# Optimization experiments

Measured on AMD Instinct MI355X. Metric: run time of the kernel, lower is better.

The kernel has to match this reference:

```python
import jax, jax.numpy as jnp
import numpy as np

MEMORY_SIZE = 32768
FEATURE_DIM = 128
BATCH = 4096


def setup_inputs() -> dict:
    key = jax.random.key(0)
    k1, k2, k3, k4 = jax.random.split(key, 4)
    memory = jax.random.normal(k1, (MEMORY_SIZE, FEATURE_DIM), dtype=jnp.float32)
    input_data = jax.random.normal(k2, (BATCH, FEATURE_DIM), dtype=jnp.float32)
    write_weights = jax.random.uniform(k3, (BATCH, MEMORY_SIZE), dtype=jnp.float32)
    query = jax.random.normal(k4, (BATCH, FEATURE_DIM), dtype=jnp.float32)
    return {"memory": memory, "input_data": input_data,
            "write_weights": write_weights, "query": query}


def reference(memory, input_data, write_weights, query):
    # ---- write(): row-normalize weights, scatter-accumulate into memory ----
    # The original python double-loop computes update[j] += w[i,j] * x[i],
    # i.e. update = w_norm.T @ x  -- a single GEMM.
    w_norm = write_weights / jnp.sum(write_weights, axis=1, keepdims=True)
    update = jnp.einsum('bm,bf->mf', w_norm, input_data)  # [M, F]
    memory_new = memory + update

    # ---- read(): softmax attention over memory slots ----
    scores = jnp.matmul(query, memory_new.T)              # [B, M]
    attention_weights = jax.nn.softmax(scores, axis=1)
    retrieved_memory = jnp.matmul(attention_weights, memory_new)  # [B, F]
    confidence_scores = jnp.max(attention_weights, axis=1)        # [B]
    return retrieved_memory, confidence_scores, memory_new
```

## Files before the change

kernel.cpp:

```cpp
#include <hip/hip_runtime.h>
#include <hip/hip_bf16.h>
#include <math.h>

#define MEMSZ 32768
#define FDIM  128
#define BATCH 4096

typedef float f32x4 __attribute__((ext_vector_type(4)));
typedef _Float16 f16x8 __attribute__((ext_vector_type(8)));
typedef short bf16x8 __attribute__((ext_vector_type(8)));
typedef unsigned short u16t;
typedef unsigned int u32t;

static __device__ __forceinline__ u16t f2h_bits(float f) {
    union { _Float16 h; u16t u; } c;
    c.h = (_Float16)f;
    return c.u;
}

#define GLDS16(gsrc, ldst) \
  __builtin_amdgcn_global_load_lds((const __attribute__((address_space(1))) void*)(gsrc), \
                                   (__attribute__((address_space(3))) void*)(ldst), 16, 0, 0)

__global__ __launch_bounds__(256) void k_rowsum(const float* __restrict__ W,
                                                float* __restrict__ inv_s) {
    const int row = blockIdx.x;
    const float4* Wr = reinterpret_cast<const float4*>(W + (size_t)row * MEMSZ);
    float acc = 0.f;
    #pragma unroll 4
    for (int i = threadIdx.x; i < MEMSZ / 4; i += 256) {
        float4 v = Wr[i];
        acc += (v.x + v.y) + (v.z + v.w);
    }
    #pragma unroll
    for (int off = 32; off > 0; off >>= 1)
        acc += __shfl_down(acc, off, 64);
    __shared__ float wsum[4];
    const int lane = threadIdx.x & 63, wid = threadIdx.x >> 6;
    if (lane == 0) wsum[wid] = acc;
    __syncthreads();
    if (threadIdx.x == 0)
        inv_s[row] = 1.0f / (wsum[0] + wsum[1] + wsum[2] + wsum[3]);
}

__global__ __launch_bounds__(256) void k_prep(const float* __restrict__ X,
                                              const float* __restrict__ inv_s,
                                              u16t* __restrict__ XT) {
    __shared__ float xs[32][132];
    const int b0 = blockIdx.x * 32;
    const int tid = threadIdx.x;
    #pragma unroll
    for (int i = 0; i < 4; ++i) {
        const int idx = tid + i * 256;
        const int row = idx >> 5, c4 = idx & 31;
        const float s = inv_s[b0 + row];
        float4 v = *reinterpret_cast<const float4*>(&X[(size_t)(b0 + row) * FDIM + c4 * 4]);
        v.x *= s; v.y *= s; v.z *= s; v.w *= s;
        *reinterpret_cast<float4*>(&xs[row][c4 * 4]) = v;
    }
    __syncthreads();
    const int f = tid >> 1, half = tid & 1;
    u32t pk[8];
    #pragma unroll
    for (int h = 0; h < 8; ++h) {
        const float lo = xs[half * 16 + 2 * h][f];
        const float hi = xs[half * 16 + 2 * h + 1][f];
        asm("v_cvt_pk_bf16_f32 %0, %1, %2" : "=v"(pk[h]) : "v"(lo), "v"(hi));
    }
    uint4* dst = reinterpret_cast<uint4*>(XT + (size_t)f * BATCH + b0 + half * 16);
    dst[0] = make_uint4(pk[0], pk[1], pk[2], pk[3]);
    dst[1] = make_uint4(pk[4], pk[5], pk[6], pk[7]);
}

#define K2B 64
#define K2M 128
__global__ __launch_bounds__(512, 2) void k_update_mfma(
    const float* __restrict__ W, const u16t* __restrict__ XT,
    const float* __restrict__ Mem, float* __restrict__ MemNew,
    u16t* __restrict__ MemH, u16t* __restrict__ MemHT)
{
    __shared__ __align__(16) unsigned char wt[2][32768];

    const int tid = threadIdx.x;
    const int lane = tid & 63, w = tid >> 6;
    const int q16 = lane & 15, g = lane >> 4;
    const int wm = w >> 1, wf = w & 1;
    const int mblk = blockIdx.x * K2M;

    f32x4 acc[2][4];
    #pragma unroll
    for (int mf = 0; mf < 2; ++mf)
        #pragma unroll
        for (int ff = 0; ff < 4; ++ff) acc[mf][ff] = (f32x4){0.f, 0.f, 0.f, 0.f};

    auto stage = [&](int buf, int t) {
        const int b0 = t * K2B;
        #pragma unroll
        for (int c = 0; c < 4; ++c) {
            const int gi = c * 512 + tid;
            const int b = gi >> 5;
            const int wb = (gi & 31) * 16;
            const int m4 = wb ^ ((b & 8) << 3);
            GLDS16((const unsigned char*)W + (size_t)(b0 + b) * (MEMSZ * 4) + (size_t)mblk * 4 + m4,
                   &wt[buf][gi * 16]);
        }
    };
    auto loadB = [&](bf16x8 (&br)[4][2], int t) {
        const int b0 = t * K2B;
        #pragma unroll
        for (int ff = 0; ff < 4; ++ff)
            #pragma unroll
            for (int ks = 0; ks < 2; ++ks)
                br[ff][ks] = *reinterpret_cast<const bf16x8*>(
                    XT + (size_t)(wf * 64 + ff * 16 + q16) * BATCH + b0 + ks * 32 + g * 8);
    };
    auto compute = [&](int buf, bf16x8 (&br)[4][2]) {
        bf16x8 afr[2][2];
        const unsigned char* tb = &wt[buf][0];
        const int bm4 = (wm * 32 + q16) * 4;
        #pragma unroll
        for (int mf = 0; mf < 2; ++mf) {
            #pragma unroll
            for (int ks = 0; ks < 2; ++ks) {
                float av[8];
                #pragma unroll
                for (int e = 0; e < 8; ++e)
                    av[e] = *reinterpret_cast<const float*>(
                        tb + (ks * 32 + g * 8 + e) * 512 + ((bm4 + mf * 64) ^ ((g & 1) << 6)));
                union { u32t u[4]; bf16x8 v; } cv;
                #pragma unroll
                for (int h = 0; h < 4; ++h)
                    asm("v_cvt_pk_bf16_f32 %0, %1, %2" : "=v"(cv.u[h]) : "v"(av[2 * h]), "v"(av[2 * h + 1]));
                afr[mf][ks] = cv.v;
            }
        }
        #pragma unroll
        for (int mf = 0; mf < 2; ++mf)
            #pragma unroll
            for (int ff = 0; ff < 4; ++ff)
                #pragma unroll
                for (int ks = 0; ks < 2; ++ks)
                    acc[mf][ff] = __builtin_amdgcn_mfma_f32_16x16x32_bf16(
                        afr[mf][ks], br[ff][ks], acc[mf][ff], 0, 0, 0);
    };

    bf16x8 bE[4][2], bO[4][2];
    stage(0, 0); loadB(bE, 0);
    __syncthreads();
    const int NT = BATCH / K2B;
    for (int t = 0; t < NT; t += 2) {
        stage(1, t + 1); loadB(bO, t + 1);
        compute(0, bE);
        __syncthreads();
        if (t + 2 < NT) { stage(0, t + 2); loadB(bE, t + 2); }
        compute(1, bO);
        __syncthreads();
    }

    #pragma unroll
    for (int mf = 0; mf < 2; ++mf) {
        #pragma unroll
        for (int ff = 0; ff < 4; ++ff) {
            const int m0 = mblk + wm * 32 + mf * 16 + g * 4;
            const int fcol = wf * 64 + ff * 16 + q16;
            ushort4 ht;
            u16t* htp = reinterpret_cast<u16t*>(&ht);
            #pragma unroll
            for (int r = 0; r < 4; ++r) {
                const size_t idx = (size_t)(m0 + r) * FDIM + fcol;
                const float v = acc[mf][ff][r] + Mem[idx];
                MemNew[idx] = v;
                const u16t hb = f2h_bits(v);
                MemH[idx] = hb;
                htp[r] = hb;
            }
            *reinterpret_cast<ushort4*>(&MemHT[(size_t)fcol * MEMSZ + m0]) = ht;
        }
    }
}

#define K2_IT 16
#define K2_MT 64
__global__ __launch_bounds__(256) void k_update_f32(const float* __restrict__ W,
                                                    const float* __restrict__ X,
                                                    const float* __restrict__ inv_s,
                                                    const float* __restrict__ Mem,
                                                    float* __restrict__ MemNew) {
    __shared__ float w_lds[2][K2_IT][K2_MT];
    __shared__ float x_lds[2][K2_IT][FDIM];
    const int j0 = blockIdx.x * K2_MT;
    const int tid = threadIdx.x;
    const int tf = tid & 15;
    const int tj = tid >> 4;

    float acc[4][8];
    #pragma unroll
    for (int a = 0; a < 4; ++a)
        #pragma unroll
        for (int b = 0; b < 8; ++b) acc[a][b] = 0.f;

    float4 pw, px0, px1;
    float ps0, ps1;
    const int wr = tid >> 4, wc4 = tid & 15;
    const int xr0 = tid >> 5, xc0 = tid & 31;
    const int xr1 = (tid + 256) >> 5, xc1 = tid & 31;

    auto load_tile = [&](int it) {
        const int i0 = it * K2_IT;
        pw  = *reinterpret_cast<const float4*>(&W[(size_t)(i0 + wr) * MEMSZ + j0 + wc4 * 4]);
        px0 = *reinterpret_cast<const float4*>(&X[(size_t)(i0 + xr0) * FDIM + xc0 * 4]);
        ps0 = inv_s[i0 + xr0];
        px1 = *reinterpret_cast<const float4*>(&X[(size_t)(i0 + xr1) * FDIM + xc1 * 4]);
        ps1 = inv_s[i0 + xr1];
    };
    auto write_tile = [&](int buf) {
        *reinterpret_cast<float4*>(&w_lds[buf][wr][wc4 * 4]) = pw;
        float4 v = px0; v.x *= ps0; v.y *= ps0; v.z *= ps0; v.w *= ps0;
        *reinterpret_cast<float4*>(&x_lds[buf][xr0][xc0 * 4]) = v;
        float4 u = px1; u.x *= ps1; u.y *= ps1; u.z *= ps1; u.w *= ps1;
        *reinterpret_cast<float4*>(&x_lds[buf][xr1][xc1 * 4]) = u;
    };

    load_tile(0);
    write_tile(0);
    __syncthreads();
    const int NT = BATCH / K2_IT;
    for (int it = 0; it < NT; ++it) {
        const int cur = it & 1;
        if (it + 1 < NT) load_tile(it + 1);
        #pragma unroll 4
        for (int i = 0; i < K2_IT; ++i) {
            const float4 wv = *reinterpret_cast<const float4*>(&w_lds[cur][i][tj * 4]);
            const float4 xa = *reinterpret_cast<const float4*>(&x_lds[cur][i][tf * 4]);
            const float4 xb = *reinterpret_cast<const float4*>(&x_lds[cur][i][tf * 4 + 64]);
            const float wj[4] = {wv.x, wv.y, wv.z, wv.w};
            #pragma unroll
            for (int a = 0; a < 4; ++a) {
                acc[a][0] += wj[a] * xa.x; acc[a][1] += wj[a] * xa.y;
                acc[a][2] += wj[a] * xa.z; acc[a][3] += wj[a] * xa.w;
                acc[a][4] += wj[a] * xb.x; acc[a][5] += wj[a] * xb.y;
                acc[a][6] += wj[a] * xb.z; acc[a][7] += wj[a] * xb.w;
            }
        }
        if (it + 1 < NT) write_tile(cur ^ 1);
        __syncthreads();
    }
    #pragma unroll
    for (int a = 0; a < 4; ++a) {
        const size_t j = (size_t)j0 + tj * 4 + a;
        const float4 m0 = *reinterpret_cast<const float4*>(&Mem[j * FDIM + tf * 4]);
        const float4 m1 = *reinterpret_cast<const float4*>(&Mem[j * FDIM + tf * 4 + 64]);
        float4 o0 = {acc[a][0] + m0.x, acc[a][1] + m0.y, acc[a][2] + m0.z, acc[a][3] + m0.w};
        float4 o1 = {acc[a][4] + m1.x, acc[a][5] + m1.y, acc[a][6] + m1.z, acc[a][7] + m1.w};
        *reinterpret_cast<float4*>(&MemNew[j * FDIM + tf * 4]) = o0;
        *reinterpret_cast<float4*>(&MemNew[j * FDIM + tf * 4 + 64]) = o1;
    }
}

__global__ __launch_bounds__(256) void k_attn_mfma(
    const float* __restrict__ Q, const u16t* __restrict__ Kh, const u16t* __restrict__ KhT,
    float* __restrict__ accP, float* __restrict__ mP, float* __restrict__ lP, int s_shift)
{
    __shared__ __align__(16) unsigned char kv_u8[2][16384];
    __shared__ __align__(16) unsigned char v_u8[2][16384];
    __shared__ __align__(16) unsigned char p_u8[4][2048];

    const int tid = threadIdx.x;
    const int w = tid >> 6, lane = tid & 63;
    const int q16 = lane & 15, g = lane >> 4;
    const int S = 1 << s_shift;
    const int s_idx = blockIdx.x & (S - 1);
    const int qb = blockIdx.x >> s_shift;
    const int chunk = MEMSZ >> s_shift;
    const int slot0 = s_idx * chunk;
    const int NT = chunk >> 6;

    f16x8 qfrag[2][4];
    #pragma unroll
    for (int qf = 0; qf < 2; ++qf) {
        const float* qrow = Q + (size_t)(qb * 128 + w * 32 + qf * 16 + q16) * FDIM;
        #pragma unroll
        for (int ks = 0; ks < 4; ++ks) {
            float tmp[8];
            *reinterpret_cast<float4*>(&tmp[0]) = *reinterpret_cast<const float4*>(&qrow[ks * 32 + g * 8]);
            *reinterpret_cast<float4*>(&tmp[4]) = *reinterpret_cast<const float4*>(&qrow[ks * 32 + g * 8 + 4]);
            f16x8 v;
            #pragma unroll
            for (int e = 0; e < 8; ++e) v[e] = (_Float16)tmp[e];
            qfrag[qf][ks] = v;
        }
    }

    auto stage = [&](int buf, int tile) {
        const unsigned char* kbase = (const unsigned char*)Kh + (size_t)(slot0 + tile * 64) * 256;
        const unsigned char* tbase = (const unsigned char*)KhT + (size_t)(slot0 + tile * 64) * 2;
        #pragma unroll
        for (int c = 0; c < 4; ++c) {
            const int C = w * 4 + c;
            const int pp = C * 1024 + lane * 16;
            {
                const int slot = pp >> 8;
                const int inner = (pp & 255) ^ ((slot & 7) << 4);
                GLDS16(kbase + slot * 256 + inner, &kv_u8[buf][C * 1024]);
            }
            {
                const int d = pp >> 7;
                const int inner = (pp & 127) ^ ((d & 7) << 4);
                GLDS16(tbase + (size_t)d * 65536 + inner, &v_u8[buf][C * 1024]);
            }
        }
    };

    float m_run[2] = {-3.0e38f, -3.0e38f};
    float l_run[2] = {0.f, 0.f};
    f32x4 acc_o[8][2];
    #pragma unroll
    for (int df = 0; df < 8; ++df)
        #pragma unroll
        for (int qf = 0; qf < 2; ++qf)
            acc_o[df][qf] = (f32x4){0.f, 0.f, 0.f, 0.f};

    stage(0, 0);
    asm volatile("s_waitcnt vmcnt(0)" ::: "memory");
    __builtin_amdgcn_s_barrier();
    __builtin_amdgcn_sched_barrier(0);

    int cur = 0;
    for (int t = 0; t < NT; ++t) {
        if (t + 1 < NT) stage(cur ^ 1, t + 1);

        f32x4 acc_s[4][2];
        #pragma unroll
        for (int sf = 0; sf < 4; ++sf) {
            acc_s[sf][0] = (f32x4){0.f, 0.f, 0.f, 0.f};
            acc_s[sf][1] = (f32x4){0.f, 0.f, 0.f, 0.f};
        }
        const unsigned char* kvb = &kv_u8[cur][0];
        #pragma unroll
        for (int ks = 0; ks < 4; ++ks) {
            #pragma unroll
            for (int sf = 0; sf < 4; ++sf) {
                const int slot = sf * 16 + q16;
                const f16x8 a = *reinterpret_cast<const f16x8*>(
                    kvb + slot * 256 + ((ks * 64 + g * 16) ^ ((slot & 7) << 4)));
                acc_s[sf][0] = __builtin_amdgcn_mfma_f32_16x16x32_f16(a, qfrag[0][ks], acc_s[sf][0], 0, 0, 0);
                acc_s[sf][1] = __builtin_amdgcn_mfma_f32_16x16x32_f16(a, qfrag[1][ks], acc_s[sf][1], 0, 0, 0);
            }
        }

        f16x8 pb[2][2];
        unsigned char* pw = &p_u8[w][0];
        #pragma unroll
        for (int qf = 0; qf < 2; ++qf) {
            float pmax = acc_s[0][qf][0];
            #pragma unroll
            for (int sf = 0; sf < 4; ++sf)
                #pragma unroll
                for (int r = 0; r < 4; ++r)
                    pmax = fmaxf(pmax, acc_s[sf][qf][r]);
            pmax = fmaxf(pmax, __shfl_xor(pmax, 16));
            pmax = fmaxf(pmax, __shfl_xor(pmax, 32));
            const float mn = fmaxf(m_run[qf], pmax);
            float p[4][4];
            float psum = 0.f;
            #pragma unroll
            for (int sf = 0; sf < 4; ++sf)
                #pragma unroll
                for (int r = 0; r < 4; ++r) {
                    p[sf][r] = __expf(acc_s[sf][qf][r] - mn);
                    psum += p[sf][r];
                }
            psum += __shfl_xor(psum, 16);
            psum += __shfl_xor(psum, 32);
            const float sc = __expf(m_run[qf] - mn);
            l_run[qf] = l_run[qf] * sc + psum;
            m_run[qf] = mn;
            #pragma unroll
            for (int df = 0; df < 8; ++df) {
                acc_o[df][qf][0] *= sc; acc_o[df][qf][1] *= sc;
                acc_o[df][qf][2] *= sc; acc_o[df][qf][3] *= sc;
            }
            #pragma unroll
            for (int sf = 0; sf < 4; ++sf)
                #pragma unroll
                for (int rr = 0; rr < 2; ++rr) {
                    const u32t val = (u32t)f2h_bits(p[sf][2 * rr]) | ((u32t)f2h_bits(p[sf][2 * rr + 1]) << 16);
                    const int byte = q16 * 128 + (((sf * 16 + g * 4 + 2 * rr) * 2) ^ ((q16 & 7) << 4));
                    *reinterpret_cast<u32t*>(pw + byte) = val;
                }
            #pragma unroll
            for (int kk = 0; kk < 2; ++kk) {
                const int byte = q16 * 128 + (((kk * 32 + g * 8) * 2) ^ ((q16 & 7) << 4));
                pb[qf][kk] = *reinterpret_cast<const f16x8*>(pw + byte);
            }
        }

        const unsigned char* vb = &v_u8[cur][0];
        #pragma unroll
        for (int df = 0; df < 8; ++df) {
            #pragma unroll
            for (int kk = 0; kk < 2; ++kk) {
                const int d = df * 16 + q16;
                const f16x8 av = *reinterpret_cast<const f16x8*>(
                    vb + d * 128 + ((kk * 64 + g * 16) ^ ((d & 7) << 4)));
                acc_o[df][0] = __builtin_amdgcn_mfma_f32_16x16x32_f16(av, pb[0][kk], acc_o[df][0], 0, 0, 0);
                acc_o[df][1] = __builtin_amdgcn_mfma_f32_16x16x32_f16(av, pb[1][kk], acc_o[df][1], 0, 0, 0);
            }
        }

        asm volatile("s_waitcnt vmcnt(0)" ::: "memory");
        __builtin_amdgcn_s_barrier();
        __builtin_amdgcn_sched_barrier(0);
        cur ^= 1;
    }

    const int rowbase = qb * 128 + w * 32;
    #pragma unroll
    for (int qf = 0; qf < 2; ++qf) {
        const int row = rowbase + qf * 16 + q16;
        float* ap = accP + ((size_t)s_idx * BATCH + row) * FDIM;
        #pragma unroll
        for (int df = 0; df < 8; ++df) {
            float4 o = {acc_o[df][qf][0], acc_o[df][qf][1], acc_o[df][qf][2], acc_o[df][qf][3]};
            *reinterpret_cast<float4*>(&ap[df * 16 + g * 4]) = o;
        }
        if (g == 0) {
            mP[(size_t)s_idx * BATCH + row] = m_run[qf];
            lP[(size_t)s_idx * BATCH + row] = l_run[qf];
        }
    }
}

__global__ __launch_bounds__(256) void k_combine(const float* __restrict__ mP,
                                                 const float* __restrict__ lP,
                                                 const float* __restrict__ accP,
                                                 float* __restrict__ Out,
                                                 float* __restrict__ Conf, int S) {
    const int row = blockIdx.x * 8 + (threadIdx.x >> 5);
    const int lane = threadIdx.x & 31;
    float mt = -3.0e38f;
    for (int s = 0; s < S; ++s) mt = fmaxf(mt, mP[(size_t)s * BATCH + row]);
    float lt = 0.f;
    for (int s = 0; s < S; ++s) lt += lP[(size_t)s * BATCH + row] * __expf(mP[(size_t)s * BATCH + row] - mt);
    const float inv = 1.0f / lt;
    float4 o = {0.f, 0.f, 0.f, 0.f};
    for (int s = 0; s < S; ++s) {
        const float wgt = __expf(mP[(size_t)s * BATCH + row] - mt);
        const float4 a = *reinterpret_cast<const float4*>(&accP[((size_t)s * BATCH + row) * FDIM + lane * 4]);
        o.x += wgt * a.x; o.y += wgt * a.y; o.z += wgt * a.z; o.w += wgt * a.w;
    }
    float4 res = {o.x * inv, o.y * inv, o.z * inv, o.w * inv};
    *reinterpret_cast<float4*>(&Out[(size_t)row * FDIM + lane * 4]) = res;
    if (lane == 0) Conf[row] = inv;
}

#define QT 16
#define MT 64
#define LSTR (FDIM + 4)
__global__ __launch_bounds__(256) void k_attn_f32(const float* __restrict__ Q,
                                                  const float* __restrict__ MemNew,
                                                  float* __restrict__ Out,
                                                  float* __restrict__ Conf) {
    __shared__ float mem_lds[MT][LSTR];
    __shared__ float q_lds[QT][LSTR];
    __shared__ float p_lds[QT][MT];
    __shared__ float m_lds[QT], l_lds[QT], scale_lds[QT];

    const int tid = threadIdx.x;
    const int qblk = blockIdx.x * QT;

    #pragma unroll
    for (int r = 0; r < 2; ++r) {
        const int idx = tid + r * 256;
        const int row = idx >> 5, c4 = idx & 31;
        *reinterpret_cast<float4*>(&q_lds[row][c4 * 4]) =
            *reinterpret_cast<const float4*>(&Q[(size_t)(qblk + row) * FDIM + c4 * 4]);
    }
    if (tid < QT) { m_lds[tid] = -3.0e38f; l_lds[tid] = 0.f; }

    const int sq = (tid >> 5) * 2;
    const int sm = tid & 31;
    const int pq = tid >> 4;
    const int pf = (tid & 15) * 4;

    float acc[8];
    #pragma unroll
    for (int e = 0; e < 8; ++e) acc[e] = 0.f;

    for (int mt = 0; mt < MEMSZ / MT; ++mt) {
        __syncthreads();
        const float* src = MemNew + (size_t)mt * MT * FDIM;
        #pragma unroll
        for (int r = 0; r < 8; ++r) {
            const int idx = tid + r * 256;
            const int row = idx >> 5, c4 = idx & 31;
            *reinterpret_cast<float4*>(&mem_lds[row][c4 * 4]) =
                *reinterpret_cast<const float4*>(&src[(size_t)row * FDIM + c4 * 4]);
        }
        const float mold0 = m_lds[sq], mold1 = m_lds[sq + 1];
        __syncthreads();

        float s00 = 0.f, s01 = 0.f, s10 = 0.f, s11 = 0.f;
        #pragma unroll 8
        for (int k = 0; k < FDIM; k += 4) {
            const float4 qa = *reinterpret_cast<const float4*>(&q_lds[sq][k]);
            const float4 qb = *reinterpret_cast<const float4*>(&q_lds[sq + 1][k]);
            const float4 ma = *reinterpret_cast<const float4*>(&mem_lds[sm][k]);
            const float4 mb = *reinterpret_cast<const float4*>(&mem_lds[sm + 32][k]);
            s00 += qa.x*ma.x + qa.y*ma.y + qa.z*ma.z + qa.w*ma.w;
            s01 += qa.x*mb.x + qa.y*mb.y + qa.z*mb.z + qa.w*mb.w;
            s10 += qb.x*ma.x + qb.y*ma.y + qb.z*ma.z + qb.w*ma.w;
            s11 += qb.x*mb.x + qb.y*mb.y + qb.z*mb.z + qb.w*mb.w;
        }
        float r0 = fmaxf(s00, s01), r1 = fmaxf(s10, s11);
        #pragma unroll
        for (int off = 1; off <= 16; off <<= 1) {
            r0 = fmaxf(r0, __shfl_xor(r0, off, 64));
            r1 = fmaxf(r1, __shfl_xor(r1, off, 64));
        }
        const float mn0 = fmaxf(mold0, r0), mn1 = fmaxf(mold1, r1);
        const float p00 = __expf(s00 - mn0), p01 = __expf(s01 - mn0);
        const float p10 = __expf(s10 - mn1), p11 = __expf(s11 - mn1);
        float t0 = p00 + p01, t1 = p10 + p11;
        #pragma unroll
        for (int off = 1; off <= 16; off <<= 1) {
            t0 += __shfl_xor(t0, off, 64);
            t1 += __shfl_xor(t1, off, 64);
        }
        p_lds[sq][sm]      = p00; p_lds[sq][sm + 32]     = p01;
        p_lds[sq + 1][sm]  = p10; p_lds[sq + 1][sm + 32] = p11;
        if (sm == 0) {
            const float sc0 = __expf(mold0 - mn0), sc1 = __expf(mold1 - mn1);
            m_lds[sq] = mn0; m_lds[sq + 1] = mn1;
            l_lds[sq]     = l_lds[sq]     * sc0 + t0;
            l_lds[sq + 1] = l_lds[sq + 1] * sc1 + t1;
            scale_lds[sq] = sc0; scale_lds[sq + 1] = sc1;
        }
        __syncthreads();

        const float sc = scale_lds[pq];
        #pragma unroll
        for (int e = 0; e < 8; ++e) acc[e] *= sc;
        #pragma unroll 8
        for (int m = 0; m < MT; ++m) {
            const float p = p_lds[pq][m];
            const float4 va = *reinterpret_cast<const float4*>(&mem_lds[m][pf]);
            const float4 vb = *reinterpret_cast<const float4*>(&mem_lds[m][pf + 64]);
            acc[0] += p * va.x; acc[1] += p * va.y; acc[2] += p * va.z; acc[3] += p * va.w;
            acc[4] += p * vb.x; acc[5] += p * vb.y; acc[6] += p * vb.z; acc[7] += p * vb.w;
        }
    }
    const float linv = 1.0f / l_lds[pq];
    float4 o0 = {acc[0]*linv, acc[1]*linv, acc[2]*linv, acc[3]*linv};
    float4 o1 = {acc[4]*linv, acc[5]*linv, acc[6]*linv, acc[7]*linv};
    *reinterpret_cast<float4*>(&Out[(size_t)(qblk + pq) * FDIM + pf]) = o0;
    *reinterpret_cast<float4*>(&Out[(size_t)(qblk + pq) * FDIM + pf + 64]) = o1;
    if (tid < QT) Conf[qblk + tid] = 1.0f / l_lds[tid];
}

extern "C" void kernel_launch(void* const* d_in, const int* in_sizes, int n_in,
                              void* d_out, int out_size, void* d_ws, size_t ws_size,
                              hipStream_t stream) {
    (void)in_sizes; (void)n_in; (void)out_size;
    const float* memory   = (const float*)d_in[0];
    const float* input    = (const float*)d_in[1];
    const float* wweights = (const float*)d_in[2];
    const float* query    = (const float*)d_in[3];

    float* out       = (float*)d_out;
    float* retrieved = out;
    float* conf      = out + (size_t)BATCH * FDIM;
    float* mem_new   = conf + BATCH;

    char* ws = (char*)d_ws;
    float* inv_s = (float*)ws;
    const size_t off_xt   = 16384;
    const size_t off_h    = off_xt + (size_t)FDIM * BATCH * 2;
    const size_t off_hT   = off_h + (size_t)MEMSZ * FDIM * 2;
    const size_t off_part = off_hT + (size_t)MEMSZ * FDIM * 2;

    int s_shift = -1;
    for (int sh = 4; sh >= 0; --sh) {
        const size_t S = (size_t)1 << sh;
        const size_t need = off_part + S * ((size_t)BATCH * 8 + (size_t)BATCH * FDIM * 4);
        if (ws_size >= need) { s_shift = sh; break; }
    }

    k_rowsum<<<BATCH, 256, 0, stream>>>(wweights, inv_s);
    if (s_shift >= 0) {
        const int S = 1 << s_shift;
        u16t* xt  = (u16t*)(ws + off_xt);
        u16t* mh  = (u16t*)(ws + off_h);
        u16t* mhT = (u16t*)(ws + off_hT);
        float* mP   = (float*)(ws + off_part);
        float* lP   = mP + (size_t)S * BATCH;
        float* accP = lP + (size_t)S * BATCH;
        k_prep<<<BATCH / 32, 256, 0, stream>>>(input, inv_s, xt);
        k_update_mfma<<<MEMSZ / K2M, 512, 0, stream>>>(wweights, xt, memory, mem_new, mh, mhT);
        k_attn_mfma<<<(BATCH / 128) * S, 256, 0, stream>>>(query, mh, mhT, accP, mP, lP, s_shift);
        k_combine<<<BATCH / 8, 256, 0, stream>>>(mP, lP, accP, retrieved, conf, S);
    } else {
        k_update_f32<<<MEMSZ / K2_MT, 256, 0, stream>>>(wweights, input, inv_s, memory, mem_new);
        k_attn_f32<<<BATCH / QT, 256, 0, stream>>>(query, mem_new, retrieved, conf);
    }
}
```

Baseline: 468.9 us.

## Triple-buffer weight staging and pre-swizzle X into MFMA fragment layout

The prep kernel now writes the normalized input in a tile-blocked layout that matches the MFMA B-fragment order, so each lane loads contiguous 16-byte chunks instead of strided rows. The update GEMM moves from two to three LDS buffers, issuing the async global-to-LDS copy two tiles ahead. It replaces __syncthreads with raw s_barrier plus explicit vmcnt waits so loads stay in flight across compute. LDS use grows to 96KB per block, which may cut occupancy from the requested two blocks per CU, and the hand-counted vmcnt values must exactly match the number of outstanding loads.

Result: faster. 407.7 us (-13.0%).

```diff
diff --git a/kernel.cpp b/kernel.cpp
--- a/kernel.cpp
+++ b/kernel.cpp
@@ -45,12 +45,13 @@
 
 __global__ __launch_bounds__(256) void k_prep(const float* __restrict__ X,
                                               const float* __restrict__ inv_s,
-                                              u16t* __restrict__ XT) {
-    __shared__ float xs[32][132];
-    const int b0 = blockIdx.x * 32;
+                                              unsigned char* __restrict__ XT64) {
+    __shared__ float xs[64][132];
+    const int T = blockIdx.x;
+    const int b0 = T * 64;
     const int tid = threadIdx.x;
     #pragma unroll
-    for (int i = 0; i < 4; ++i) {
+    for (int i = 0; i < 8; ++i) {
         const int idx = tid + i * 256;
         const int row = idx >> 5, c4 = idx & 31;
         const float s = inv_s[b0 + row];
@@ -59,27 +60,32 @@
         *reinterpret_cast<float4*>(&xs[row][c4 * 4]) = v;
     }
     __syncthreads();
-    const int f = tid >> 1, half = tid & 1;
-    u32t pk[8];
-    #pragma unroll
-    for (int h = 0; h < 8; ++h) {
-        const float lo = xs[half * 16 + 2 * h][f];
-        const float hi = xs[half * 16 + 2 * h + 1][f];
-        asm("v_cvt_pk_bf16_f32 %0, %1, %2" : "=v"(pk[h]) : "v"(lo), "v"(hi));
-    }
-    uint4* dst = reinterpret_cast<uint4*>(XT + (size_t)f * BATCH + b0 + half * 16);
-    dst[0] = make_uint4(pk[0], pk[1], pk[2], pk[3]);
-    dst[1] = make_uint4(pk[4], pk[5], pk[6], pk[7]);
+    #pragma unroll
+    for (int i = 0; i < 4; ++i) {
+        const int L = tid + i * 256;
+        const int fh = L >> 9, ff = (L >> 7) & 3, ks = (L >> 6) & 1, ln = L & 63;
+        const int f = fh * 64 + ff * 16 + (ln & 15);
+        const int bi = ks * 32 + (ln >> 4) * 8;
+        u32t pk[4];
+        #pragma unroll
+        for (int h = 0; h < 4; ++h) {
+            const float lo = xs[bi + 2 * h][f];
+            const float hi = xs[bi + 2 * h + 1][f];
+            asm("v_cvt_pk_bf16_f32 %0, %1, %2" : "=v"(pk[h]) : "v"(lo), "v"(hi));
+        }
+        *reinterpret_cast<uint4*>(XT64 + (size_t)T * 16384 + (size_t)L * 16) =
+            make_uint4(pk[0], pk[1], pk[2], pk[3]);
+    }
 }
 
 #define K2B 64
 #define K2M 128
 __global__ __launch_bounds__(512, 2) void k_update_mfma(
-    const float* __restrict__ W, const u16t* __restrict__ XT,
+    const float* __restrict__ W, const unsigned char* __restrict__ XT64,
     const float* __restrict__ Mem, float* __restrict__ MemNew,
     u16t* __restrict__ MemH, u16t* __restrict__ MemHT)
 {
-    __shared__ __align__(16) unsigned char wt[2][32768];
+    __shared__ __align__(16) unsigned char wt[3][32768];
 
     const int tid = threadIdx.x;
     const int lane = tid & 63, w = tid >> 6;
@@ -93,7 +99,7 @@
         #pragma unroll
         for (int ff = 0; ff < 4; ++ff) acc[mf][ff] = (f32x4){0.f, 0.f, 0.f, 0.f};
 
-    auto stage = [&](int buf, int t) {
+    auto stageW = [&](int buf, int t) {
         const int b0 = t * K2B;
         #pragma unroll
         for (int c = 0; c < 4; ++c) {
@@ -106,17 +112,16 @@
         }
     };
     auto loadB = [&](bf16x8 (&br)[4][2], int t) {
-        const int b0 = t * K2B;
+        const unsigned char* base = XT64 + (size_t)t * 16384 + wf * 8192 + lane * 16;
         #pragma unroll
         for (int ff = 0; ff < 4; ++ff)
             #pragma unroll
             for (int ks = 0; ks < 2; ++ks)
-                br[ff][ks] = *reinterpret_cast<const bf16x8*>(
-                    XT + (size_t)(wf * 64 + ff * 16 + q16) * BATCH + b0 + ks * 32 + g * 8);
+                br[ff][ks] = *reinterpret_cast<const bf16x8*>(base + ff * 2048 + ks * 1024);
     };
     auto compute = [&](int buf, bf16x8 (&br)[4][2]) {
         bf16x8 afr[2][2];
-        const unsigned char* tb = &wt[buf][0];
+        const unsigned char* tb = &wt[0][0] + buf * 32768;
         const int bm4 = (wm * 32 + q16) * 4;
         #pragma unroll
         for (int mf = 0; mf < 2; ++mf) {
@@ -144,17 +149,30 @@
                         afr[mf][ks], br[ff][ks], acc[mf][ff], 0, 0, 0);
     };
 
-    bf16x8 bE[4][2], bO[4][2];
-    stage(0, 0); loadB(bE, 0);
-    __syncthreads();
+    bf16x8 bA[4][2], bB_[4][2];
+    stageW(0, 0); stageW(1, 1); loadB(bA, 0);
     const int NT = BATCH / K2B;
     for (int t = 0; t < NT; t += 2) {
-        stage(1, t + 1); loadB(bO, t + 1);
-        compute(0, bE);
-        __syncthreads();
-        if (t + 2 < NT) { stage(0, t + 2); loadB(bE, t + 2); }
-        compute(1, bO);
-        __syncthreads();
+        __builtin_amdgcn_s_barrier();
+        if (t + 2 < NT) stageW((t + 2) % 3, t + 2);
+        if (t + 1 < NT) loadB(bB_, t + 1);
+        if (t + 2 < NT)      asm volatile("s_waitcnt vmcnt(16)" ::: "memory");
+        else if (t + 1 < NT) asm volatile("s_waitcnt vmcnt(12)" ::: "memory");
+        else                 asm volatile("s_waitcnt vmcnt(0)"  ::: "memory");
+        __builtin_amdgcn_s_barrier();
+        __builtin_amdgcn_sched_barrier(0);
+        compute(t % 3, bA);
+        if (t + 1 < NT) {
+            __builtin_amdgcn_s_barrier();
+            if (t + 3 < NT) stageW((t + 3) % 3, t + 3);
+            if (t + 2 < NT) loadB(bA, t + 2);
+            if (t + 3 < NT)      asm volatile("s_waitcnt vmcnt(16)" ::: "memory");
+            else if (t + 2 < NT) asm volatile("s_waitcnt vmcnt(12)" ::: "memory");
+            else                 asm volatile("s_waitcnt vmcnt(0)"  ::: "memory");
+            __builtin_amdgcn_s_barrier();
+            __builtin_amdgcn_sched_barrier(0);
+            compute((t + 1) % 3, bB_);
+        }
     }
 
     #pragma unroll
@@ -589,14 +607,14 @@
     k_rowsum<<<BATCH, 256, 0, stream>>>(wweights, inv_s);
     if (s_shift >= 0) {
         const int S = 1 << s_shift;
-        u16t* xt  = (u16t*)(ws + off_xt);
+        unsigned char* xt64 = (unsigned char*)(ws + off_xt);
         u16t* mh  = (u16t*)(ws + off_h);
         u16t* mhT = (u16t*)(ws + off_hT);
         float* mP   = (float*)(ws + off_part);
         float* lP   = mP + (size_t)S * BATCH;
         float* accP = lP + (size_t)S * BATCH;
-        k_prep<<<BATCH / 32, 256, 0, stream>>>(input, inv_s, xt);
-        k_update_mfma<<<MEMSZ / K2M, 512, 0, stream>>>(wweights, xt, memory, mem_new, mh, mhT);
+        k_prep<<<BATCH / 64, 256, 0, stream>>>(input, inv_s, xt64);
+        k_update_mfma<<<MEMSZ / K2M, 512, 0, stream>>>(wweights, xt64, memory, mem_new, mh, mhT);
         k_attn_mfma<<<(BATCH / 128) * S, 256, 0, stream>>>(query, mh, mhT, accP, mP, lP, s_shift);
         k_combine<<<BATCH / 8, 256, 0, stream>>>(mP, lP, accP, retrieved, conf, S);
     } else {
```
